# Kernel optimization log

Hardware: AMD Instinct MI355X
Metric: run time of the kernel (lower is better)

Reference implementation:

```python
import jax, jax.numpy as jnp
import numpy as np

B, S, C, E = 4, 4096, 256, 256  # batch, seq, in_channel, embedding_dim


def setup_inputs() -> dict:
    key = jax.random.key(0)
    ks = jax.random.split(key, 7)
    scale = 1.0 / np.sqrt(C)
    return {
        "x": jax.random.normal(ks[0], (B, S, C), dtype=jnp.float32),
        "Wq": jax.random.uniform(ks[1], (C, C), jnp.float32, -scale, scale),
        "bq": jax.random.uniform(ks[2], (C,), jnp.float32, -scale, scale),
        "Wk": jax.random.uniform(ks[3], (C, C), jnp.float32, -scale, scale),
        "bk": jax.random.uniform(ks[4], (C,), jnp.float32, -scale, scale),
        "Wv": jax.random.uniform(ks[5], (C, E), jnp.float32, -scale, scale),
        "bv": jax.random.uniform(ks[6], (E,), jnp.float32, -scale, scale),
    }


def reference(x, Wq, bq, Wk, bk, Wv, bv):
    # QKV projections (weights stored as [in, out])
    Q = jnp.einsum("bsc,cd->bsd", x, Wq) + bq  # [B,S,C]
    K = jnp.einsum("bsc,cd->bsd", x, Wk) + bk  # [B,S,C]
    V = jnp.einsum("bsc,ce->bse", x, Wv) + bv  # [B,S,E]
    # Unscaled attention scores, softmax over keys
    scores = jnp.einsum("bqc,bkc->bqk", Q, K)  # [B,S,S]
    attn = jax.nn.softmax(scores, axis=-1)
    attended = jnp.einsum("bqk,bke->bqe", attn, V)  # [B,S,E]
    # Dropout(0.5) treated as identity (eval mode)
    return jax.nn.sigmoid(attended)
```

## Files before the change

### kernel.cpp

```cpp
#include <hip/hip_runtime.h>
#include <cstdint>
#include <cstddef>

#define DI __device__ __forceinline__

typedef __bf16 bf16x8 __attribute__((ext_vector_type(8)));
typedef _Float16 f16x8 __attribute__((ext_vector_type(8)));
typedef float f32x4 __attribute__((ext_vector_type(4)));

constexpr int Bb = 4, Ss = 4096, Cc = 256, Ee = 256;

constexpr size_t OFF_Q   = 786432;
constexpr size_t OFF_K   = 9175040;
constexpr size_t OFF_V   = 17563648;
constexpr size_t OFF_PML = 25952256;

DI unsigned bf_hi(float f) {
  unsigned u = __builtin_bit_cast(unsigned, f);
  return (u + 0x7fffu + ((u >> 16) & 1u)) >> 16;
}
DI float bf_f(unsigned h) { return __builtin_bit_cast(float, h << 16); }

DI unsigned cvtpk(float a, float b) {
  unsigned r;
  asm("v_cvt_pk_bf16_f32 %0, %1, %2" : "=v"(r) : "v"(a), "v"(b));
  return r;
}
DI void split4(float4 v, uint2& h, uint2& l) {
  unsigned h01 = cvtpk(v.x, v.y), h23 = cvtpk(v.z, v.w);
  float e0 = __builtin_bit_cast(float, h01 << 16);
  float e1 = __builtin_bit_cast(float, h01 & 0xffff0000u);
  float e2 = __builtin_bit_cast(float, h23 << 16);
  float e3 = __builtin_bit_cast(float, h23 & 0xffff0000u);
  h = make_uint2(h01, h23);
  l = make_uint2(cvtpk(v.x - e0, v.y - e1), cvtpk(v.z - e2, v.w - e3));
}
DI unsigned short f16b(float v) {
  _Float16 h = (_Float16)v;
  return __builtin_bit_cast(unsigned short, h);
}
DI unsigned pkf16(float a, float b) {
  return __builtin_bit_cast(unsigned, __builtin_amdgcn_cvt_pkrtz(a, b));
}

DI f32x4 mfma16(bf16x8 a, bf16x8 b, f32x4 c) {
  return __builtin_amdgcn_mfma_f32_16x16x32_bf16(a, b, c, 0, 0, 0);
}
DI f32x4 mfma16f(f16x8 a, f16x8 b, f32x4 c) {
  return __builtin_amdgcn_mfma_f32_16x16x32_f16(a, b, c, 0, 0, 0);
}

DI void gl16(const void* g, void* l) {
  __builtin_amdgcn_global_load_lds(
      (const __attribute__((address_space(1))) unsigned*)g,
      (__attribute__((address_space(3))) unsigned*)l, 16, 0, 0);
}


__global__ __launch_bounds__(256) void k_transpose(
    const float* __restrict__ wq, const float* __restrict__ wk,
    const float* __restrict__ wv, float* __restrict__ wt) {
  const float* src = blockIdx.x == 0 ? wq : (blockIdx.x == 1 ? wk : wv);
  float* dst = wt + (size_t)blockIdx.x * Cc * Cc;
  const int n = threadIdx.x;
  for (int k = 0; k < Cc; k++) dst[n * Cc + k] = src[k * Cc + n];
}

__global__ __launch_bounds__(256, 2) void k_proj(
    const float* __restrict__ x, const float* __restrict__ wt,
    const float* __restrict__ bq, const float* __restrict__ bk,
    const float* __restrict__ bv, char* __restrict__ ws) {
  __shared__ __align__(16) unsigned short xh[64 * 64], xl[64 * 64];
  __shared__ __align__(16) unsigned short wh[64 * 64], wl[64 * 64];
  const int t = threadIdx.x, lane = t & 63, wid = t >> 6;
  const int mat = blockIdx.z;
  const int n0 = blockIdx.y * 64, m0 = blockIdx.x * 64;
  const float* wm = wt + (size_t)mat * Cc * Cc;
  const float* bias = mat == 0 ? bq : (mat == 1 ? bk : bv);

  f32x4 acc[4];
#pragma unroll
  for (int f = 0; f < 4; f++) acc[f] = (f32x4){0.f, 0.f, 0.f, 0.f};

  const int srow = t >> 2, scol = (t & 3) * 16;

  for (int k0 = 0; k0 < Cc; k0 += 64) {
    const float* xs = x + (size_t)(m0 + srow) * Cc + k0 + scol;
    const float* wsrc = wm + (size_t)(n0 + srow) * Cc + k0 + scol;
#pragma unroll
    for (int j = 0; j < 16; j += 4) {
      const int off = srow * 128 + (((scol + j) * 2) ^ ((srow & 7) << 4));
      uint2 h, l;
      split4(*(const float4*)(xs + j), h, l);
      *(uint2*)((char*)xh + off) = h;
      *(uint2*)((char*)xl + off) = l;
      split4(*(const float4*)(wsrc + j), h, l);
      *(uint2*)((char*)wh + off) = h;
      *(uint2*)((char*)wl + off) = l;
    }
    __syncthreads();
#pragma unroll
    for (int c2 = 0; c2 < 2; c2++) {
      const int arow = wid * 16 + (lane & 15);
      const int aby = arow * 128 + ((c2 * 64 + (lane >> 4) * 16) ^ ((arow & 7) << 4));
      bf16x8 ah = *(const bf16x8*)((const char*)xh + aby);
      bf16x8 al = *(const bf16x8*)((const char*)xl + aby);
#pragma unroll
      for (int f = 0; f < 4; f++) {
        const int brow = f * 16 + (lane & 15);
        const int bby = brow * 128 + ((c2 * 64 + (lane >> 4) * 16) ^ ((brow & 7) << 4));
        bf16x8 bh = *(const bf16x8*)((const char*)wh + bby);
        bf16x8 bl = *(const bf16x8*)((const char*)wl + bby);
        acc[f] = mfma16(ah, bh, acc[f]);
        acc[f] = mfma16(al, bh, acc[f]);
        acc[f] = mfma16(ah, bl, acc[f]);
      }
    }
    __syncthreads();
  }

  const int mgbase = m0 + wid * 16 + (lane >> 4) * 4;
#pragma unroll
  for (int f = 0; f < 4; f++) {
    const int ncol = n0 + f * 16 + (lane & 15);
    const float bb = bias[ncol];
    if (mat == 0) {
      unsigned short* qd = (unsigned short*)(ws + OFF_Q);
#pragma unroll
      for (int r = 0; r < 4; r++) {
        const int mg = mgbase + r;
        qd[(size_t)mg * Cc + ncol] = f16b(acc[f][r] + bb);
      }
    } else if (mat == 1) {
      char* kf = ws + OFF_K;
#pragma unroll
      for (int r = 0; r < 4; r++) {
        const int mg = mgbase + r;
        const int bidx = mg >> 12, sg = mg & 4095;
        const int kt = sg >> 5, krow = sg & 31;
        const size_t base = ((size_t)(bidx * 128 + kt)) * 16384 +
                            (size_t)(krow * 512 + ((ncol * 2) ^ ((krow & 7) << 4)));
        *(unsigned short*)(kf + base) = f16b(acc[f][r] + bb);
      }
    } else {
      char* vf = ws + OFF_V;
      unsigned short h[4];
#pragma unroll
      for (int r = 0; r < 4; r++) h[r] = f16b(acc[f][r] + bb);
      const int mg = mgbase;
      const int bidx = mg >> 12, sg = mg & 4095;
      const int kt = sg >> 5, kin = sg & 31;
      const int e = ncol;
      const size_t img = (size_t)((e >> 1) * 128 +
                         (((e & 1) * 64 + kin * 2) ^ (((e >> 1) & 7) << 4)));
      *(uint2*)(vf + ((size_t)(bidx * 128 + kt)) * 16384 + img) =
          make_uint2((unsigned)h[0] | ((unsigned)h[1] << 16),
                     (unsigned)h[2] | ((unsigned)h[3] << 16));
    }
  }
}

__global__ __launch_bounds__(256, 2) void k_attn(
    char* __restrict__ ws, float* __restrict__ out, int nz) {
  __shared__ __align__(16) char sbuf[36864];
  const int t = threadIdx.x, lane = t & 63, w = t >> 6;
  const int qt = blockIdx.x, b = blockIdx.y, z = blockIdx.z;
  const int q0 = qt * 64;
  const int ktq = 128 / nz, ktr = 128 % nz;
  const int kt0 = z * ktq + (z < ktr ? z : ktr);
  const int cnt = ktq + (z < ktr ? 1 : 0);

  f16x8 qf[8];
  {
    const int qrow = q0 + w * 16 + (lane & 15);
    const unsigned short* qp =
        (const unsigned short*)(ws + OFF_Q) + (size_t)(b * Ss + qrow) * Cc;
#pragma unroll
    for (int c = 0; c < 8; c++)
      qf[c] = *(const f16x8*)(qp + c * 32 + (lane >> 4) * 8);
  }

  unsigned srcoff[8];
#pragma unroll
  for (int j = 0; j < 8; j++) {
    const int L = w * 8192 + j * 1024;
    const unsigned rb = (L < 16384) ? (unsigned)OFF_K : (unsigned)OFF_V;
    srcoff[j] = rb + (unsigned)b * 2097152u + (unsigned)kt0 * 16384u +
                (unsigned)(L & 16383) + (unsigned)(lane * 16);
  }

  f32x4 acc[16];
#pragma unroll
  for (int eg = 0; eg < 16; eg++) acc[eg] = (f32x4){0.f, 0.f, 0.f, 0.f};
  float mrun[4] = {-1e30f, -1e30f, -1e30f, -1e30f};
  float lrun[4] = {0.f, 0.f, 0.f, 0.f};

#pragma unroll
  for (int j = 0; j < 8; j++) gl16(ws + srcoff[j], sbuf + w * 8192 + j * 1024);
  __syncthreads();

  char* const phb = sbuf + 32768 + w * 1024;

  for (int it = 0; it < cnt; it++) {
    f32x4 sacc[2];
    sacc[0] = (f32x4){0.f, 0.f, 0.f, 0.f};
    sacc[1] = (f32x4){0.f, 0.f, 0.f, 0.f};
    __builtin_amdgcn_s_setprio(1);
#pragma unroll
    for (int c = 0; c < 8; c++) {
#pragma unroll
      for (int f = 0; f < 2; f++) {
        const int krow = f * 16 + (lane & 15);
        const int kby = krow * 512 + ((c * 64 + (lane >> 4) * 16) ^ ((krow & 7) << 4));
        sacc[f] = mfma16f(qf[c], *(const f16x8*)(sbuf + kby), sacc[f]);
      }
    }
    __builtin_amdgcn_s_setprio(0);

    float tm[4];
#pragma unroll
    for (int r = 0; r < 4; r++) tm[r] = fmaxf(sacc[0][r], sacc[1][r]);
#pragma unroll
    for (int r = 0; r < 4; r++) {
      tm[r] = fmaxf(tm[r], __shfl_xor(tm[r], 1, 64));
      tm[r] = fmaxf(tm[r], __shfl_xor(tm[r], 2, 64));
      tm[r] = fmaxf(tm[r], __shfl_xor(tm[r], 4, 64));
      tm[r] = fmaxf(tm[r], __shfl_xor(tm[r], 8, 64));
    }
    int ok = 1;
#pragma unroll
    for (int r = 0; r < 4; r++) ok &= (tm[r] <= mrun[r] + 5.5f) ? 1 : 0;
    if (!__all(ok)) {
      float sc[4];
#pragma unroll
      for (int r = 0; r < 4; r++) {
        float mn = fmaxf(mrun[r], tm[r]);
        sc[r] = __expf(mrun[r] - mn);
        mrun[r] = mn;
        lrun[r] *= sc[r];
      }
#pragma unroll
      for (int eg = 0; eg < 16; eg++) {
        acc[eg][0] *= sc[0]; acc[eg][1] *= sc[1];
        acc[eg][2] *= sc[2]; acc[eg][3] *= sc[3];
      }
    }
    float rsum[4] = {0.f, 0.f, 0.f, 0.f};
#pragma unroll
    for (int f = 0; f < 2; f++) {
#pragma unroll
      for (int r = 0; r < 4; r++) {
        float p = __expf(sacc[f][r] - mrun[r]);
        sacc[f][r] = p;
        rsum[r] += p;
      }
    }
#pragma unroll
    for (int r = 0; r < 4; r++) {
      rsum[r] += __shfl_xor(rsum[r], 1, 64);
      rsum[r] += __shfl_xor(rsum[r], 2, 64);
      rsum[r] += __shfl_xor(rsum[r], 4, 64);
      rsum[r] += __shfl_xor(rsum[r], 8, 64);
      lrun[r] += rsum[r];
    }

#pragma unroll
    for (int r = 0; r < 4; r++) {
      const unsigned wpk = pkf16(sacc[0][r], sacc[1][r]);
      const int q = (lane >> 4) * 4 + r;
      const int c0 = (lane & 15) * 2;
      const int lineb = (q >> 1) * 128, sw = ((q >> 1) & 7) << 4, half = (q & 1) * 64;
      *(unsigned short*)(phb + lineb + ((half + c0) ^ sw)) = (unsigned short)wpk;
      *(unsigned short*)(phb + lineb + ((half + 32 + c0) ^ sw)) =
          (unsigned short)(wpk >> 16);
    }

    {
      const int q = lane & 15;
      const int pby = (q >> 1) * 128 +
                      (((q & 1) * 64 + (lane >> 4) * 16) ^ (((q >> 1) & 7) << 4));
      f16x8 pa = *(const f16x8*)(phb + pby);
      __builtin_amdgcn_s_setprio(1);
#pragma unroll
      for (int eg = 0; eg < 16; eg++) {
        const int erow = eg * 16 + (lane & 15);
        const int vby = (erow >> 1) * 128 +
                        (((erow & 1) * 64 + (lane >> 4) * 16) ^ (((erow >> 1) & 7) << 4));
        acc[eg] = mfma16f(pa, *(const f16x8*)(sbuf + 16384 + vby), acc[eg]);
      }
      __builtin_amdgcn_s_setprio(0);
    }

    __syncthreads();
    if (it + 1 < cnt) {
#pragma unroll
      for (int j = 0; j < 8; j++) {
        srcoff[j] += 16384;
        gl16(ws + srcoff[j], sbuf + w * 8192 + j * 1024);
      }
    }
    __syncthreads();
  }

  const int qloc0 = w * 16 + (lane >> 4) * 4;
  if (z == 0) {
#pragma unroll
    for (int eg = 0; eg < 16; eg++) {
      const int e = eg * 16 + (lane & 15);
#pragma unroll
      for (int r = 0; r < 4; r++)
        out[((size_t)(b * Ss + q0 + qloc0 + r)) * Ee + e] = acc[eg][r];
    }
  } else {
    unsigned short* p1 = (unsigned short*)(ws + OFF_PML + (size_t)nz * 131072 +
                                           (size_t)(z - 1) * 8388608);
#pragma unroll
    for (int eg = 0; eg < 16; eg++) {
      const int e = eg * 16 + (lane & 15);
#pragma unroll
      for (int r = 0; r < 4; r++)
        p1[((size_t)((b * 64 + qt) * 64 + qloc0 + r)) * 256 + e] =
            (unsigned short)bf_hi(acc[eg][r]);
    }
  }
  if ((lane & 15) == 0) {
    float* pml = (float*)(ws + OFF_PML);
#pragma unroll
    for (int r = 0; r < 4; r++) {
      const int q = qloc0 + r;
      pml[(((size_t)(z * 4 + b) * 64 + qt) * 2 + 0) * 64 + q] = mrun[r];
      pml[(((size_t)(z * 4 + b) * 64 + qt) * 2 + 1) * 64 + q] = lrun[r];
    }
  }
}

__global__ __launch_bounds__(256) void k_comb(
    char* __restrict__ ws, float* __restrict__ out, int nz) {
  __shared__ float sm[3][16], sl[3][16];
  const int t = threadIdx.x, qt = blockIdx.x, b = blockIdx.y, qz = blockIdx.z;
  const float* pml = (const float*)(ws + OFF_PML);
  if (t < 16 * nz) {
    const int z = t >> 4, qq = t & 15;
    const int q = qz * 16 + qq;
    sm[z][qq] = pml[(((size_t)(z * 4 + b) * 64 + qt) * 2 + 0) * 64 + q];
    sl[z][qq] = pml[(((size_t)(z * 4 + b) * 64 + qt) * 2 + 1) * 64 + q];
  }
  __syncthreads();
  const unsigned short* p1 =
      (const unsigned short*)(ws + OFF_PML + (size_t)nz * 131072);
  for (int qi = 0; qi < 16; qi++) {
    const int q = qz * 16 + qi;
    const size_t o = ((size_t)(b * Ss + qt * 64 + q)) * Ee + t;
    float M = sm[0][qi];
    for (int z = 1; z < nz; z++) M = fmaxf(M, sm[z][qi]);
    float a0 = __expf(sm[0][qi] - M);
    float num = out[o] * a0, den = sl[0][qi] * a0;
    for (int z = 1; z < nz; z++) {
      float az = __expf(sm[z][qi] - M);
      float oz = bf_f(p1[(size_t)(z - 1) * 4194304 +
                         ((size_t)((b * 64 + qt) * 64 + q)) * 256 + t]);
      num += oz * az;
      den += sl[z][qi] * az;
    }
    float v = num / den;
    out[o] = 1.f / (1.f + __expf(-v));
  }
}

extern "C" void kernel_launch(void* const* d_in, const int* in_sizes, int n_in,
                              void* d_out, int out_size, void* d_ws, size_t ws_size,
                              hipStream_t stream) {
  (void)in_sizes; (void)n_in; (void)out_size; (void)ws_size;
  const float* x  = (const float*)d_in[0];
  const float* Wq = (const float*)d_in[1];
  const float* bq = (const float*)d_in[2];
  const float* Wk = (const float*)d_in[3];
  const float* bk = (const float*)d_in[4];
  const float* Wv = (const float*)d_in[5];
  const float* bv = (const float*)d_in[6];
  float* out = (float*)d_out;
  char* ws = (char*)d_ws;
  float* wt = (float*)ws;

  const int nz = 3;

  hipLaunchKernelGGL(k_transpose, dim3(3), dim3(256), 0, stream, Wq, Wk, Wv, wt);
  hipLaunchKernelGGL(k_proj, dim3(256, 4, 3), dim3(256), 0, stream,
                     x, wt, bq, bk, bv, ws);
  hipLaunchKernelGGL(k_attn, dim3(64, Bb, nz), dim3(256), 0, stream, ws, out, nz);
  hipLaunchKernelGGL(k_comb, dim3(64, Bb, 4), dim3(256), 0, stream, ws, out, nz);
}
```

Before: 280.4 us.

## Use fp16 weight image for projection, register-staged K/V prefetch, four-way key split

The QKV projection drops the three-MFMA split-bf16 scheme in favour of a single fp16 MFMA. It reads a pre-swizzled fp16 weight image that a new tiled LDS transpose kernel builds, and converts x to fp16 in registers with no LDS staging. The attention kernel now loads the next K/V tile into registers at the start of each iteration and writes it to LDS after the barrier, replacing global_load_lds issued after the compute. The key dimension is split four ways instead of three to put more blocks in flight, at the cost of more partial-result traffic in the combine kernel. Projection accuracy drops from near-fp32 to fp16, and the extra register staging may raise register pressure in the attention kernel.

```diff
diff --git a/kernel.cpp b/kernel.cpp
--- a/kernel.cpp
+++ b/kernel.cpp
@@ -4,12 +4,12 @@
 
 #define DI __device__ __forceinline__
 
-typedef __bf16 bf16x8 __attribute__((ext_vector_type(8)));
 typedef _Float16 f16x8 __attribute__((ext_vector_type(8)));
 typedef float f32x4 __attribute__((ext_vector_type(4)));
 
 constexpr int Bb = 4, Ss = 4096, Cc = 256, Ee = 256;
 
+constexpr size_t OFF_W   = 0;
 constexpr size_t OFF_Q   = 786432;
 constexpr size_t OFF_K   = 9175040;
 constexpr size_t OFF_V   = 17563648;
@@ -20,32 +20,18 @@
   return (u + 0x7fffu + ((u >> 16) & 1u)) >> 16;
 }
 DI float bf_f(unsigned h) { return __builtin_bit_cast(float, h << 16); }
-
-DI unsigned cvtpk(float a, float b) {
-  unsigned r;
-  asm("v_cvt_pk_bf16_f32 %0, %1, %2" : "=v"(r) : "v"(a), "v"(b));
-  return r;
-}
-DI void split4(float4 v, uint2& h, uint2& l) {
-  unsigned h01 = cvtpk(v.x, v.y), h23 = cvtpk(v.z, v.w);
-  float e0 = __builtin_bit_cast(float, h01 << 16);
-  float e1 = __builtin_bit_cast(float, h01 & 0xffff0000u);
-  float e2 = __builtin_bit_cast(float, h23 << 16);
-  float e3 = __builtin_bit_cast(float, h23 & 0xffff0000u);
-  h = make_uint2(h01, h23);
-  l = make_uint2(cvtpk(v.x - e0, v.y - e1), cvtpk(v.z - e2, v.w - e3));
-}
 DI unsigned short f16b(float v) {
   _Float16 h = (_Float16)v;
   return __builtin_bit_cast(unsigned short, h);
 }
+DI unsigned pk16rne(float a, float b) {
+  return (unsigned)f16b(a) | ((unsigned)f16b(b) << 16);
+}
 DI unsigned pkf16(float a, float b) {
   return __builtin_bit_cast(unsigned, __builtin_amdgcn_cvt_pkrtz(a, b));
 }
-
-DI f32x4 mfma16(bf16x8 a, bf16x8 b, f32x4 c) {
-  return __builtin_amdgcn_mfma_f32_16x16x32_bf16(a, b, c, 0, 0, 0);
-}
+DI float uf(unsigned u) { return __builtin_bit_cast(float, u); }
+
 DI f32x4 mfma16f(f16x8 a, f16x8 b, f32x4 c) {
   return __builtin_amdgcn_mfma_f32_16x16x32_f16(a, b, c, 0, 0, 0);
 }
@@ -59,78 +45,78 @@
 
 __global__ __launch_bounds__(256) void k_transpose(
     const float* __restrict__ wq, const float* __restrict__ wk,
-    const float* __restrict__ wv, float* __restrict__ wt) {
-  const float* src = blockIdx.x == 0 ? wq : (blockIdx.x == 1 ? wk : wv);
-  float* dst = wt + (size_t)blockIdx.x * Cc * Cc;
-  const int n = threadIdx.x;
-  for (int k = 0; k < Cc; k++) dst[n * Cc + k] = src[k * Cc + n];
+    const float* __restrict__ wv, char* __restrict__ wimg_all) {
+  __shared__ float lds[64][65];
+  const int t = threadIdx.x;
+  const int kt = blockIdx.x, nt = blockIdx.y, mat = blockIdx.z;
+  const float* src = mat == 0 ? wq : (mat == 1 ? wk : wv);
+#pragma unroll
+  for (int i = 0; i < 16; i++) {
+    const int kr = i * 4 + (t >> 6);
+    lds[kr][t & 63] = src[(size_t)(kt * 64 + kr) * Cc + nt * 64 + (t & 63)];
+  }
+  __syncthreads();
+  char* wimg = wimg_all + (size_t)mat * 131072 + (size_t)kt * 32768;
+  const int nl = t >> 2, qd = t & 3;
+  const int n = nt * 64 + nl;
+#pragma unroll
+  for (int h = 0; h < 2; h++) {
+    const int kl = qd * 16 + h * 8;
+    uint4 pk = make_uint4(pk16rne(lds[kl + 0][nl], lds[kl + 1][nl]),
+                          pk16rne(lds[kl + 2][nl], lds[kl + 3][nl]),
+                          pk16rne(lds[kl + 4][nl], lds[kl + 5][nl]),
+                          pk16rne(lds[kl + 6][nl], lds[kl + 7][nl]));
+    *(uint4*)(wimg + n * 128 + ((qd * 32 + h * 16) ^ ((n & 7) << 4))) = pk;
+  }
 }
 
 __global__ __launch_bounds__(256, 2) void k_proj(
-    const float* __restrict__ x, const float* __restrict__ wt,
-    const float* __restrict__ bq, const float* __restrict__ bk,
-    const float* __restrict__ bv, char* __restrict__ ws) {
-  __shared__ __align__(16) unsigned short xh[64 * 64], xl[64 * 64];
-  __shared__ __align__(16) unsigned short wh[64 * 64], wl[64 * 64];
-  const int t = threadIdx.x, lane = t & 63, wid = t >> 6;
-  const int mat = blockIdx.z;
-  const int n0 = blockIdx.y * 64, m0 = blockIdx.x * 64;
-  const float* wm = wt + (size_t)mat * Cc * Cc;
+    const float* __restrict__ x, const float* __restrict__ bq,
+    const float* __restrict__ bk, const float* __restrict__ bv,
+    char* __restrict__ ws) {
+  const int t = threadIdx.x, lane = t & 63, w = t >> 6;
+  const int m0 = blockIdx.x * 64, mat = blockIdx.y;
   const float* bias = mat == 0 ? bq : (mat == 1 ? bk : bv);
-
-  f32x4 acc[4];
-#pragma unroll
-  for (int f = 0; f < 4; f++) acc[f] = (f32x4){0.f, 0.f, 0.f, 0.f};
-
-  const int srow = t >> 2, scol = (t & 3) * 16;
-
-  for (int k0 = 0; k0 < Cc; k0 += 64) {
-    const float* xs = x + (size_t)(m0 + srow) * Cc + k0 + scol;
-    const float* wsrc = wm + (size_t)(n0 + srow) * Cc + k0 + scol;
-#pragma unroll
-    for (int j = 0; j < 16; j += 4) {
-      const int off = srow * 128 + (((scol + j) * 2) ^ ((srow & 7) << 4));
-      uint2 h, l;
-      split4(*(const float4*)(xs + j), h, l);
-      *(uint2*)((char*)xh + off) = h;
-      *(uint2*)((char*)xl + off) = l;
-      split4(*(const float4*)(wsrc + j), h, l);
-      *(uint2*)((char*)wh + off) = h;
-      *(uint2*)((char*)wl + off) = l;
-    }
-    __syncthreads();
+  const char* wimg = ws + OFF_W + (size_t)mat * 131072;
+
+  f32x4 acc[16];
+#pragma unroll
+  for (int f = 0; f < 16; f++) acc[f] = (f32x4){0.f, 0.f, 0.f, 0.f};
+
+  const int mrow = m0 + w * 16 + (lane & 15);
+  const float* xrow = x + (size_t)mrow * Cc;
+
+  for (int k0t = 0; k0t < 4; k0t++) {
+    const char* wk0 = wimg + k0t * 32768;
 #pragma unroll
     for (int c2 = 0; c2 < 2; c2++) {
-      const int arow = wid * 16 + (lane & 15);
-      const int aby = arow * 128 + ((c2 * 64 + (lane >> 4) * 16) ^ ((arow & 7) << 4));
-      bf16x8 ah = *(const bf16x8*)((const char*)xh + aby);
-      bf16x8 al = *(const bf16x8*)((const char*)xl + aby);
-#pragma unroll
-      for (int f = 0; f < 4; f++) {
-        const int brow = f * 16 + (lane & 15);
-        const int bby = brow * 128 + ((c2 * 64 + (lane >> 4) * 16) ^ ((brow & 7) << 4));
-        bf16x8 bh = *(const bf16x8*)((const char*)wh + bby);
-        bf16x8 bl = *(const bf16x8*)((const char*)wl + bby);
-        acc[f] = mfma16(ah, bh, acc[f]);
-        acc[f] = mfma16(al, bh, acc[f]);
-        acc[f] = mfma16(ah, bl, acc[f]);
-      }
-    }
-    __syncthreads();
-  }
-
-  const int mgbase = m0 + wid * 16 + (lane >> 4) * 4;
-#pragma unroll
-  for (int f = 0; f < 4; f++) {
-    const int ncol = n0 + f * 16 + (lane & 15);
+      const float* xk = xrow + k0t * 64 + c2 * 32 + (lane >> 4) * 8;
+      uint4 a0 = *(const uint4*)(xk);
+      uint4 a1 = *(const uint4*)(xk + 4);
+      uint4 apk = make_uint4(pk16rne(uf(a0.x), uf(a0.y)),
+                             pk16rne(uf(a0.z), uf(a0.w)),
+                             pk16rne(uf(a1.x), uf(a1.y)),
+                             pk16rne(uf(a1.z), uf(a1.w)));
+      f16x8 af = __builtin_bit_cast(f16x8, apk);
+#pragma unroll
+      for (int f = 0; f < 16; f++) {
+        const int n = f * 16 + (lane & 15);
+        const int by = n * 128 + ((c2 * 64 + (lane >> 4) * 16) ^ ((n & 7) << 4));
+        acc[f] = mfma16f(af, *(const f16x8*)(wk0 + by), acc[f]);
+      }
+    }
+  }
+
+  const int mgbase = m0 + w * 16 + (lane >> 4) * 4;
+#pragma unroll
+  for (int f = 0; f < 16; f++) {
+    const int ncol = f * 16 + (lane & 15);
     const float bb = bias[ncol];
     if (mat == 0) {
       unsigned short* qd = (unsigned short*)(ws + OFF_Q);
 #pragma unroll
-      for (int r = 0; r < 4; r++) {
-        const int mg = mgbase + r;
-        qd[(size_t)mg * Cc + ncol] = f16b(acc[f][r] + bb);
-      }
+      for (int r = 0; r < 4; r++)
+        qd[(size_t)(mgbase + r) * Cc + ncol] = f16b(acc[f][r] + bb);
     } else if (mat == 1) {
       char* kf = ws + OFF_K;
 #pragma unroll
@@ -200,8 +186,16 @@
   __syncthreads();
 
   char* const phb = sbuf + 32768 + w * 1024;
+  uint4 stg[8];
 
   for (int it = 0; it < cnt; it++) {
+    const bool pf = (it + 1 < cnt);
+    if (pf) {
+#pragma unroll
+      for (int j = 0; j < 8; j++)
+        stg[j] = *(const uint4*)(ws + srcoff[j] + 16384);
+    }
+
     f32x4 sacc[2];
     sacc[0] = (f32x4){0.f, 0.f, 0.f, 0.f};
     sacc[1] = (f32x4){0.f, 0.f, 0.f, 0.f};
@@ -292,11 +286,11 @@
     }
 
     __syncthreads();
-    if (it + 1 < cnt) {
+    if (pf) {
 #pragma unroll
       for (int j = 0; j < 8; j++) {
         srcoff[j] += 16384;
-        gl16(ws + srcoff[j], sbuf + w * 8192 + j * 1024);
+        *(uint4*)(sbuf + w * 8192 + j * 1024 + lane * 16) = stg[j];
       }
     }
     __syncthreads();
@@ -336,7 +330,7 @@
 
 __global__ __launch_bounds__(256) void k_comb(
     char* __restrict__ ws, float* __restrict__ out, int nz) {
-  __shared__ float sm[3][16], sl[3][16];
+  __shared__ float sm[4][16], sl[4][16];
   const int t = threadIdx.x, qt = blockIdx.x, b = blockIdx.y, qz = blockIdx.z;
   const float* pml = (const float*)(ws + OFF_PML);
   if (t < 16 * nz) {
@@ -380,13 +374,13 @@
   const float* bv = (const float*)d_in[6];
   float* out = (float*)d_out;
   char* ws = (char*)d_ws;
-  float* wt = (float*)ws;
-
-  const int nz = 3;
-
-  hipLaunchKernelGGL(k_transpose, dim3(3), dim3(256), 0, stream, Wq, Wk, Wv, wt);
-  hipLaunchKernelGGL(k_proj, dim3(256, 4, 3), dim3(256), 0, stream,
-                     x, wt, bq, bk, bv, ws);
+
+  const int nz = 4;
+
+  hipLaunchKernelGGL(k_transpose, dim3(4, 4, 3), dim3(256), 0, stream,
+                     Wq, Wk, Wv, ws + OFF_W);
+  hipLaunchKernelGGL(k_proj, dim3(256, 3), dim3(256), 0, stream,
+                     x, bq, bk, bv, ws);
   hipLaunchKernelGGL(k_attn, dim3(64, Bb, nz), dim3(256), 0, stream, ws, out, nz);
   hipLaunchKernelGGL(k_comb, dim3(64, Bb, 4), dim3(256), 0, stream, ws, out, nz);
 }
```

After: 533.5 us. +90.3%, slower.
